# Kernel optimization log

Hardware: AMD Instinct MI355X
Metric: run time of the kernel (lower is better)

## Reference

```python
import jax, jax.numpy as jnp
import numpy as np

N_NODES = 50000
N_EDGES = 800000
F_IN = 64
H = 128
N_CLASSES = 10
NUM_GRAPHS = 512


def setup_inputs() -> dict:
    key = jax.random.key(0)
    ks = jax.random.split(key, 16)
    x = jax.random.normal(ks[0], (N_NODES, F_IN), dtype=jnp.float32)
    edge_index = jax.random.randint(ks[1], (2, N_EDGES), 0, N_NODES, dtype=jnp.int64)
    batch = jnp.sort(jax.random.randint(ks[2], (N_NODES,), 0, NUM_GRAPHS, dtype=jnp.int64))

    def lin(k, fi, fo):
        kw, kb = jax.random.split(k)
        s = 1.0 / np.sqrt(fi)
        return (jax.random.uniform(kw, (fi, fo), jnp.float32, -s, s),
                jax.random.uniform(kb, (fo,), jnp.float32, -s, s))

    W0, b0 = lin(ks[3], F_IN, H)
    W1, b1 = lin(ks[4], H, H)
    W2, b2 = lin(ks[5], H, H)
    mW0, mb0 = lin(ks[6], H, H)
    mW1, mb1 = lin(ks[7], H, H)
    mW2, mb2 = lin(ks[8], H, N_CLASSES)
    return {"x": x, "edge_index": edge_index, "batch": batch,
            "W0": W0, "b0": b0, "W1": W1, "b1": b1, "W2": W2, "b2": b2,
            "mW0": mW0, "mb0": mb0, "mW1": mW1, "mb1": mb1, "mW2": mW2, "mb2": mb2}


def reference(x, edge_index, batch, W0, b0, W1, b1, W2, b2, mW0, mb0, mW1, mb1, mW2, mb2):
    N = x.shape[0]
    loop = jnp.arange(N, dtype=edge_index.dtype)
    src = jnp.concatenate([edge_index[0], loop])  # add self-loops (PyG GCNConv)
    dst = jnp.concatenate([edge_index[1], loop])
    deg = jax.ops.segment_sum(jnp.ones_like(src, jnp.float32), dst, num_segments=N)
    dinv = jnp.where(deg > 0, deg ** -0.5, 0.0)
    norm = dinv[src] * dinv[dst]  # [E+N]

    def gcn(h, W, b):
        h = h @ W                                   # [N, H]
        msg = h[src] * norm[:, None]                # gather [E+N, H]
        return jax.ops.segment_sum(msg, dst, num_segments=N) + b

    h = jax.nn.relu(gcn(x, W0, b0))
    h = jax.nn.relu(gcn(h, W1, b1))
    h = jax.nn.relu(gcn(h, W2, b2))
    g = jax.ops.segment_sum(h, batch, num_segments=NUM_GRAPHS)  # global_add_pool
    g = jax.nn.relu(g @ mW0 + mb0)
    g = jax.nn.relu(g @ mW1 + mb1)
    return g @ mW2 + mb2  # [NUM_GRAPHS, N_CLASSES]
```

## Files before the change

### kernel.cpp

```cpp
#include <hip/hip_runtime.h>
#include <hip/hip_bf16.h>
#include <stdint.h>

#define N_NODES   50000
#define N_EDGES   800000
#define F_IN      64
#define HID       128
#define N_CLASSES 10
#define NUM_GRAPHS 512

#define NBUCK 128
#define BW    391
#define S1B   400
#define CHUNK 2000
#define MCNT  (NBUCK * S1B)
#define PREPB 3125

typedef unsigned int uint32;
typedef __attribute__((ext_vector_type(8))) short bf16x8;
typedef __attribute__((ext_vector_type(4))) float f32x4;

__device__ __forceinline__ float bl(uint32 w) { return __uint_as_float(w << 16); }
__device__ __forceinline__ float bh(uint32 w) { return __uint_as_float(w & 0xffff0000u); }
__device__ __forceinline__ uint32 packbf(float a, float b) {
    uint32 ua = __float_as_uint(a), ub = __float_as_uint(b);
    ua = (ua + 0x7fffu + ((ua >> 16) & 1u)) >> 16;
    ub = (ub + 0x7fffu + ((ub >> 16) & 1u)) >> 16;
    return ua | (ub << 16);
}
__device__ __forceinline__ unsigned short packbf1(float a) {
    uint32 ua = __float_as_uint(a);
    return (unsigned short)((ua + 0x7fffu + ((ua >> 16) & 1u)) >> 16);
}

__global__ __launch_bounds__(256) void prep_hist_kernel(const float4* __restrict__ x, uint2* __restrict__ xb,
                                                        const float* __restrict__ W0, unsigned short* __restrict__ W0t,
                                                        const float* __restrict__ W1, unsigned short* __restrict__ W1t,
                                                        const float* __restrict__ W2, unsigned short* __restrict__ W2t,
                                                        const int* __restrict__ dst, int* __restrict__ bcnt, int E) {
    __shared__ int cnt[NBUCK];
    int blk = blockIdx.x;
    int t = threadIdx.x;
    if (blk < PREPB) {
        int i = blk * 256 + t;
        if (i < N_NODES * F_IN / 4) {
            float4 v = x[i];
            xb[i] = make_uint2(packbf(v.x, v.y), packbf(v.z, v.w));
        }
        if (i < 64 * 128) {
            int k = i >> 7, j = i & 127;
            W0t[j * (64 + 8) + k] = packbf1(W0[i]);
        }
        int i2 = i - 64 * 128;
        if (i2 >= 0 && i2 < 128 * 128) {
            int k = i2 >> 7, j = i2 & 127;
            W1t[j * (128 + 8) + k] = packbf1(W1[i2]);
            W2t[j * (128 + 8) + k] = packbf1(W2[i2]);
        }
    } else {
        int b2 = blk - PREPB;
        if (t < NBUCK) cnt[t] = 0;
        __syncthreads();
        int base = b2 * CHUNK;
        for (int i = t; i < CHUNK; i += 256) {
            int e = base + i;
            if (e < E) atomicAdd(&cnt[(uint32)dst[e] / BW], 1);
        }
        __syncthreads();
        if (t < NBUCK) bcnt[t * S1B + b2] = cnt[t];
    }
}

__global__ __launch_bounds__(256) void scanA_kernel(const int* __restrict__ in,
                                                    int* __restrict__ incl,
                                                    int* __restrict__ bsum, int M) {
    __shared__ int s[256];
    int t = threadIdx.x;
    int i = blockIdx.x * 256 + t;
    int v = (i < M) ? in[i] : 0;
    s[t] = v;
    __syncthreads();
    #pragma unroll
    for (int d = 1; d < 256; d <<= 1) {
        int a = (t >= d) ? s[t - d] : 0;
        __syncthreads();
        s[t] += a;
        __syncthreads();
    }
    if (i < M) incl[i] = s[t];
    if (t == 255) bsum[blockIdx.x] = s[255];
}

__global__ __launch_bounds__(256) void scanB_kernel(int* __restrict__ bsum, int NB) {
    __shared__ int s[256];
    int t = threadIdx.x;
    int v = (t < NB) ? bsum[t] : 0;
    s[t] = v;
    __syncthreads();
    #pragma unroll
    for (int d = 1; d < 256; d <<= 1) {
        int a = (t >= d) ? s[t - d] : 0;
        __syncthreads();
        s[t] += a;
        __syncthreads();
    }
    if (t < NB) bsum[t] = s[t] - v;
}

__global__ __launch_bounds__(256) void bscatter_kernel(const int* __restrict__ src,
                                                       const int* __restrict__ dst,
                                                       const int* __restrict__ incl,
                                                       const int* __restrict__ bsum,
                                                       int2* __restrict__ ebuf, int E) {
    __shared__ int cnt[NBUCK];
    __shared__ int cur[NBUCK];
    int t = threadIdx.x, blk = blockIdx.x;
    if (t < NBUCK) cnt[t] = 0;
    __syncthreads();
    int base = blk * CHUNK;
    for (int i = t; i < CHUNK; i += 256) {
        int e = base + i;
        if (e < E) atomicAdd(&cnt[(uint32)dst[e] / BW], 1);
    }
    __syncthreads();
    if (t < NBUCK) {
        int idx = t * S1B + blk;
        cur[t] = bsum[idx >> 8] + incl[idx] - cnt[t];
    }
    __syncthreads();
    for (int i = t; i < CHUNK; i += 256) {
        int e = base + i;
        if (e < E) {
            int d = dst[e];
            int slot = atomicAdd(&cur[(uint32)d / BW], 1);
            ebuf[slot] = make_int2(src[e], d);
        }
    }
}

__global__ __launch_bounds__(256) void bfinal_kernel(const int2* __restrict__ ebuf,
                                                     const int* __restrict__ bcnt,
                                                     const int* __restrict__ incl,
                                                     const int* __restrict__ bsum,
                                                     int* __restrict__ rowptr,
                                                     float* __restrict__ dinv,
                                                     int2* __restrict__ meta, int E, int N) {
    __shared__ int cnt[392];
    __shared__ int startv[400];
    __shared__ int segt[16];
    int t = threadIdx.x, b = blockIdx.x;

    int bs, be;
    {
        int idx = b * S1B;
        bs = bsum[idx >> 8] + incl[idx] - bcnt[idx];
        if (b + 1 >= NBUCK) be = E;
        else {
            int idx1 = (b + 1) * S1B;
            be = bsum[idx1 >> 8] + incl[idx1] - bcnt[idx1];
        }
    }

    for (int i = t; i < 392; i += 256) cnt[i] = 0;
    __syncthreads();
    for (int i = bs + t; i < be; i += 256) {
        int d = ebuf[i].y;
        atomicAdd(&cnt[d - b * BW], 1);
    }
    __syncthreads();

    if (t < 16) {
        int run = 0;
        #pragma unroll
        for (int k = 0; k < 25; k++) {
            int idx = t * 25 + k;
            int c = (idx < 391) ? cnt[idx] : 0;
            startv[idx] = run;
            run += c;
        }
        segt[t] = run;
    }
    __syncthreads();
    if (t == 0) {
        int run = 0;
        #pragma unroll
        for (int j = 0; j < 16; j++) { int s = segt[j]; segt[j] = run; run += s; }
    }
    __syncthreads();
    for (int l = t; l < 391; l += 256) startv[l] += segt[l / 25] + bs;
    __syncthreads();

    int locN = N - b * BW; if (locN > BW) locN = BW;
    for (int l = t; l < locN; l += 256) {
        int g = b * BW + l;
        rowptr[g + 1] = startv[l] + cnt[l];
        dinv[g] = rsqrtf((float)(cnt[l] + 1));
    }
    if (b == 0 && t == 0) rowptr[0] = 0;
    __syncthreads();

    for (int i = bs + t; i < be; i += 256) {
        int2 sd = ebuf[i];
        int slot = atomicAdd(&startv[sd.y - b * BW], 1);
        meta[slot] = sd;
    }
}

__global__ __launch_bounds__(256) void norm_kernel(int2* __restrict__ meta,
                                                   const float* __restrict__ dinv, int E) {
    int i = blockIdx.x * 256 + threadIdx.x;
    if (i < E) {
        int2 m = meta[i];
        meta[i] = make_int2(m.x, __float_as_int(dinv[m.x] * dinv[m.y]));
    }
}

__global__ __launch_bounds__(256) void spmm128_kernel(const int* __restrict__ rowptr,
                                                      const int2* __restrict__ meta,
                                                      const float* __restrict__ dinv,
                                                      const unsigned short* __restrict__ Hin,
                                                      unsigned short* __restrict__ Hout, int N) {
    int wave = threadIdx.x >> 6;
    int lane = threadIdx.x & 63;
    int node = blockIdx.x * 4 + wave;
    if (node >= N) return;
    int q   = lane >> 4;
    int sub = lane & 15;

    const uint4* Hv = (const uint4*)Hin;
    float di = dinv[node];
    float sn = di * di;

    float acc[8];
    if (q == 0) {
        uint4 s = Hv[(size_t)node * 16 + sub];
        acc[0] = sn * bl(s.x); acc[1] = sn * bh(s.x);
        acc[2] = sn * bl(s.y); acc[3] = sn * bh(s.y);
        acc[4] = sn * bl(s.z); acc[5] = sn * bh(s.z);
        acc[6] = sn * bl(s.w); acc[7] = sn * bh(s.w);
    } else {
        #pragma unroll
        for (int v = 0; v < 8; v++) acc[v] = 0.f;
    }

    int e0 = rowptr[node];
    int e1 = rowptr[node + 1];
    for (int e = e0; e < e1; e += 16) {
        int i0 = e + q;
        int i1 = e + 4 + q;
        int i2 = e + 8 + q;
        int i3 = e + 12 + q;
        int2 m0 = (i0 < e1) ? meta[i0] : make_int2(0, 0);
        int2 m1 = (i1 < e1) ? meta[i1] : make_int2(0, 0);
        int2 m2 = (i2 < e1) ? meta[i2] : make_int2(0, 0);
        int2 m3 = (i3 < e1) ? meta[i3] : make_int2(0, 0);
        float n0 = __int_as_float(m0.y);
        float n1 = __int_as_float(m1.y);
        float n2 = __int_as_float(m2.y);
        float n3 = __int_as_float(m3.y);
        uint4 r0 = Hv[(size_t)m0.x * 16 + sub];
        uint4 r1 = Hv[(size_t)m1.x * 16 + sub];
        uint4 r2 = Hv[(size_t)m2.x * 16 + sub];
        uint4 r3 = Hv[(size_t)m3.x * 16 + sub];
        acc[0] = fmaf(n0, bl(r0.x), acc[0]); acc[1] = fmaf(n0, bh(r0.x), acc[1]);
        acc[2] = fmaf(n0, bl(r0.y), acc[2]); acc[3] = fmaf(n0, bh(r0.y), acc[3]);
        acc[4] = fmaf(n0, bl(r0.z), acc[4]); acc[5] = fmaf(n0, bh(r0.z), acc[5]);
        acc[6] = fmaf(n0, bl(r0.w), acc[6]); acc[7] = fmaf(n0, bh(r0.w), acc[7]);
        acc[0] = fmaf(n1, bl(r1.x), acc[0]); acc[1] = fmaf(n1, bh(r1.x), acc[1]);
        acc[2] = fmaf(n1, bl(r1.y), acc[2]); acc[3] = fmaf(n1, bh(r1.y), acc[3]);
        acc[4] = fmaf(n1, bl(r1.z), acc[4]); acc[5] = fmaf(n1, bh(r1.z), acc[5]);
        acc[6] = fmaf(n1, bl(r1.w), acc[6]); acc[7] = fmaf(n1, bh(r1.w), acc[7]);
        acc[0] = fmaf(n2, bl(r2.x), acc[0]); acc[1] = fmaf(n2, bh(r2.x), acc[1]);
        acc[2] = fmaf(n2, bl(r2.y), acc[2]); acc[3] = fmaf(n2, bh(r2.y), acc[3]);
        acc[4] = fmaf(n2, bl(r2.z), acc[4]); acc[5] = fmaf(n2, bh(r2.z), acc[5]);
        acc[6] = fmaf(n2, bl(r2.w), acc[6]); acc[7] = fmaf(n2, bh(r2.w), acc[7]);
        acc[0] = fmaf(n3, bl(r3.x), acc[0]); acc[1] = fmaf(n3, bh(r3.x), acc[1]);
        acc[2] = fmaf(n3, bl(r3.y), acc[2]); acc[3] = fmaf(n3, bh(r3.y), acc[3]);
        acc[4] = fmaf(n3, bl(r3.z), acc[4]); acc[5] = fmaf(n3, bh(r3.z), acc[5]);
        acc[6] = fmaf(n3, bl(r3.w), acc[6]); acc[7] = fmaf(n3, bh(r3.w), acc[7]);
    }

    #pragma unroll
    for (int v = 0; v < 8; v++) {
        acc[v] += __shfl_xor(acc[v], 16);
        acc[v] += __shfl_xor(acc[v], 32);
    }

    if (q == 0) {
        uint4 o;
        o.x = packbf(acc[0], acc[1]);
        o.y = packbf(acc[2], acc[3]);
        o.z = packbf(acc[4], acc[5]);
        o.w = packbf(acc[6], acc[7]);
        ((uint4*)Hout)[(size_t)node * 16 + sub] = o;
    }
}

__global__ __launch_bounds__(256) void spmm64_kernel(const int* __restrict__ rowptr,
                                                     const int2* __restrict__ meta,
                                                     const float* __restrict__ dinv,
                                                     const unsigned short* __restrict__ Hin,
                                                     unsigned short* __restrict__ Hout, int N) {
    int wave = threadIdx.x >> 6;
    int lane = threadIdx.x & 63;
    int node = blockIdx.x * 4 + wave;
    if (node >= N) return;
    int oct = lane >> 3;
    int sub = lane & 7;

    const uint4* Hv = (const uint4*)Hin;
    float di = dinv[node];
    float sn = di * di;

    float acc[8];
    if (oct == 0) {
        uint4 s = Hv[(size_t)node * 8 + sub];
        acc[0] = sn * bl(s.x); acc[1] = sn * bh(s.x);
        acc[2] = sn * bl(s.y); acc[3] = sn * bh(s.y);
        acc[4] = sn * bl(s.z); acc[5] = sn * bh(s.z);
        acc[6] = sn * bl(s.w); acc[7] = sn * bh(s.w);
    } else {
        #pragma unroll
        for (int v = 0; v < 8; v++) acc[v] = 0.f;
    }

    int e0 = rowptr[node];
    int e1 = rowptr[node + 1];
    for (int e = e0; e < e1; e += 16) {
        int i0 = e + oct;
        int i1 = e + 8 + oct;
        int2 m0 = (i0 < e1) ? meta[i0] : make_int2(0, 0);
        int2 m1 = (i1 < e1) ? meta[i1] : make_int2(0, 0);
        float n0 = __int_as_float(m0.y);
        float n1 = __int_as_float(m1.y);
        uint4 r0 = Hv[(size_t)m0.x * 8 + sub];
        uint4 r1 = Hv[(size_t)m1.x * 8 + sub];
        acc[0] = fmaf(n0, bl(r0.x), acc[0]); acc[1] = fmaf(n0, bh(r0.x), acc[1]);
        acc[2] = fmaf(n0, bl(r0.y), acc[2]); acc[3] = fmaf(n0, bh(r0.y), acc[3]);
        acc[4] = fmaf(n0, bl(r0.z), acc[4]); acc[5] = fmaf(n0, bh(r0.z), acc[5]);
        acc[6] = fmaf(n0, bl(r0.w), acc[6]); acc[7] = fmaf(n0, bh(r0.w), acc[7]);
        acc[0] = fmaf(n1, bl(r1.x), acc[0]); acc[1] = fmaf(n1, bh(r1.x), acc[1]);
        acc[2] = fmaf(n1, bl(r1.y), acc[2]); acc[3] = fmaf(n1, bh(r1.y), acc[3]);
        acc[4] = fmaf(n1, bl(r1.z), acc[4]); acc[5] = fmaf(n1, bh(r1.z), acc[5]);
        acc[6] = fmaf(n1, bl(r1.w), acc[6]); acc[7] = fmaf(n1, bh(r1.w), acc[7]);
    }

    #pragma unroll
    for (int v = 0; v < 8; v++) {
        acc[v] += __shfl_xor(acc[v], 8);
        acc[v] += __shfl_xor(acc[v], 16);
        acc[v] += __shfl_xor(acc[v], 32);
    }

    if (oct == 0) {
        uint4 o;
        o.x = packbf(acc[0], acc[1]);
        o.y = packbf(acc[2], acc[3]);
        o.z = packbf(acc[4], acc[5]);
        o.w = packbf(acc[6], acc[7]);
        ((uint4*)Hout)[(size_t)node * 8 + sub] = o;
    }
}

template <int K>
__global__ __launch_bounds__(256) void gemm_mfma_kernel(const unsigned short* __restrict__ A,
                                                        const unsigned short* __restrict__ Wt,
                                                        const float* __restrict__ bias,
                                                        unsigned short* __restrict__ out,
                                                        int N) {
    constexpr int KP = K + 8;
    __shared__ unsigned short Wl[128 * KP];

    int t = threadIdx.x;
    constexpr int TOT = 128 * KP * 2 / 16;
    #pragma unroll
    for (int i = 0; i < (TOT + 255) / 256; i++) {
        int idx = i * 256 + t;
        if (idx < TOT) ((uint4*)Wl)[idx] = ((const uint4*)Wt)[idx];
    }
    __syncthreads();

    int wave = t >> 6;
    int lane = t & 63;
    int rowBase = blockIdx.x * 128 + wave * 32;
    int r0 = rowBase + (lane & 15);
    int r1 = r0 + 16;
    if (r0 >= N) r0 = N - 1;
    if (r1 >= N) r1 = N - 1;
    int kchunk = lane >> 4;
    int colSub = lane & 15;

    f32x4 acc0[8], acc1[8];
    #pragma unroll
    for (int i = 0; i < 8; i++) { acc0[i] = (f32x4)0.0f; acc1[i] = (f32x4)0.0f; }

    #pragma unroll
    for (int s = 0; s < K / 32; s++) {
        bf16x8 a0 = *(const bf16x8*)(A + (size_t)r0 * K + s * 32 + kchunk * 8);
        bf16x8 a1 = *(const bf16x8*)(A + (size_t)r1 * K + s * 32 + kchunk * 8);
        #pragma unroll
        for (int tl = 0; tl < 8; tl++) {
            bf16x8 b = *(const bf16x8*)(Wl + (tl * 16 + colSub) * KP + s * 32 + kchunk * 8);
            acc0[tl] = __builtin_amdgcn_mfma_f32_16x16x32_bf16(a0, b, acc0[tl], 0, 0, 0);
            acc1[tl] = __builtin_amdgcn_mfma_f32_16x16x32_bf16(a1, b, acc1[tl], 0, 0, 0);
        }
    }

    int rowOff = (lane >> 4) * 4;
    #pragma unroll
    for (int tl = 0; tl < 8; tl++) {
        int col = tl * 16 + colSub;
        float bv = bias[col];
        #pragma unroll
        for (int r = 0; r < 4; r++) {
            int rowA = rowBase + rowOff + r;
            int rowB = rowA + 16;
            if (rowA < N) {
                float v = fmaxf(acc0[tl][r] + bv, 0.f);
                out[(size_t)rowA * 128 + col] = packbf1(v);
            }
            if (rowB < N) {
                float v = fmaxf(acc1[tl][r] + bv, 0.f);
                out[(size_t)rowB * 128 + col] = packbf1(v);
            }
        }
    }
}

__device__ __forceinline__ int lowerb(const int* a, int n, int v) {
    int lo = 0, hi = n;
    while (lo < hi) {
        int m = (lo + hi) >> 1;
        if (a[m] < v) lo = m + 1; else hi = m;
    }
    return lo;
}

__global__ __launch_bounds__(256) void pool_mlp_kernel(const unsigned short* __restrict__ H,
                                                       const int* __restrict__ batch,
                                                       const float* __restrict__ mW0, const float* __restrict__ mb0,
                                                       const float* __restrict__ mW1, const float* __restrict__ mb1,
                                                       const float* __restrict__ mW2, const float* __restrict__ mb2,
                                                       float* __restrict__ out, int N) {
    int b = blockIdx.x;
    int t = threadIdx.x;
    int jw = t & 63;
    int g  = t >> 6;
    int lo = lowerb(batch, N, b);
    int hi = lowerb(batch, N, b + 1);

    const uint32* Hu = (const uint32*)H;
    float f0 = 0.f, f1 = 0.f;
    for (int n = lo + g; n < hi; n += 4) {
        uint32 v = Hu[(size_t)n * 64 + jw];
        f0 += bl(v);
        f1 += bh(v);
    }

    __shared__ float part[4][HID];
    __shared__ float l0[HID];
    __shared__ float l1[HID];
    part[g][jw * 2 + 0] = f0;
    part[g][jw * 2 + 1] = f1;
    __syncthreads();
    if (t < 128) l0[t] = part[0][t] + part[1][t] + part[2][t] + part[3][t];
    __syncthreads();

    if (t < 128) {
        int j = t;
        float a0 = mb0[j], a1 = 0.f, a2 = 0.f, a3 = 0.f;
        #pragma unroll 4
        for (int k = 0; k < HID; k += 4) {
            a0 = fmaf(l0[k + 0], mW0[(k + 0) * HID + j], a0);
            a1 = fmaf(l0[k + 1], mW0[(k + 1) * HID + j], a1);
            a2 = fmaf(l0[k + 2], mW0[(k + 2) * HID + j], a2);
            a3 = fmaf(l0[k + 3], mW0[(k + 3) * HID + j], a3);
        }
        l1[j] = fmaxf((a0 + a1) + (a2 + a3), 0.f);
    }
    __syncthreads();

    float c = 0.f;
    if (t < 128) {
        int j = t;
        float a0 = mb1[j], a1 = 0.f, a2 = 0.f, a3 = 0.f;
        #pragma unroll 4
        for (int k = 0; k < HID; k += 4) {
            a0 = fmaf(l1[k + 0], mW1[(k + 0) * HID + j], a0);
            a1 = fmaf(l1[k + 1], mW1[(k + 1) * HID + j], a1);
            a2 = fmaf(l1[k + 2], mW1[(k + 2) * HID + j], a2);
            a3 = fmaf(l1[k + 3], mW1[(k + 3) * HID + j], a3);
        }
        c = fmaxf((a0 + a1) + (a2 + a3), 0.f);
    }
    __syncthreads();
    if (t < 128) l0[t] = c;
    __syncthreads();

    if (t < N_CLASSES) {
        float a0 = mb2[t], a1 = 0.f, a2 = 0.f, a3 = 0.f;
        #pragma unroll 4
        for (int k = 0; k < HID; k += 4) {
            a0 = fmaf(l0[k + 0], mW2[(k + 0) * N_CLASSES + t], a0);
            a1 = fmaf(l0[k + 1], mW2[(k + 1) * N_CLASSES + t], a1);
            a2 = fmaf(l0[k + 2], mW2[(k + 2) * N_CLASSES + t], a2);
            a3 = fmaf(l0[k + 3], mW2[(k + 3) * N_CLASSES + t], a3);
        }
        out[b * N_CLASSES + t] = (a0 + a1) + (a2 + a3);
    }
}

extern "C" void kernel_launch(void* const* d_in, const int* in_sizes, int n_in,
                              void* d_out, int out_size, void* d_ws, size_t ws_size,
                              hipStream_t stream) {
    const float* x     = (const float*)d_in[0];
    const int*   ei    = (const int*)d_in[1];
    const int*   batch = (const int*)d_in[2];
    const float* W0  = (const float*)d_in[3];
    const float* b0  = (const float*)d_in[4];
    const float* W1  = (const float*)d_in[5];
    const float* b1  = (const float*)d_in[6];
    const float* W2  = (const float*)d_in[7];
    const float* b2  = (const float*)d_in[8];
    const float* mW0 = (const float*)d_in[9];
    const float* mb0 = (const float*)d_in[10];
    const float* mW1 = (const float*)d_in[11];
    const float* mb1 = (const float*)d_in[12];
    const float* mW2 = (const float*)d_in[13];
    const float* mb2 = (const float*)d_in[14];
    float* out = (float*)d_out;

    const int N = N_NODES, E = N_EDGES;
    const int* src = ei;
    const int* dst = ei + E;

    char* w = (char*)d_ws;
    auto alloc = [&](size_t bytes) -> void* {
        void* p = (void*)w;
        w += (bytes + 255) & ~(size_t)255;
        return p;
    };
    int*   rowptr = (int*)alloc((size_t)(N + 1) * 4);
    int2*  ebuf   = (int2*)alloc((size_t)E * 8);
    int2*  meta   = (int2*)alloc((size_t)E * 8);
    int*   bcnt   = (int*)alloc((size_t)MCNT * 4);
    int*   incl   = (int*)alloc((size_t)MCNT * 4);
    int*   bsum   = (int*)alloc(256 * 4);
    float* dinv   = (float*)alloc((size_t)N * 4);
    unsigned short* xb   = (unsigned short*)alloc((size_t)N * F_IN * 2);
    unsigned short* bufA = (unsigned short*)alloc((size_t)N * HID * 2);
    unsigned short* bufB = (unsigned short*)alloc((size_t)N * HID * 2);
    unsigned short* W0t  = (unsigned short*)alloc((size_t)128 * (64 + 8) * 2);
    unsigned short* W1t  = (unsigned short*)alloc((size_t)128 * (128 + 8) * 2);
    unsigned short* W2t  = (unsigned short*)alloc((size_t)128 * (128 + 8) * 2);

    const int EB   = (E + 255) / 256;
    const int SPB  = (N + 3) / 4;
    const int GB   = (N + 127) / 128;
    const int SCB  = (MCNT + 255) / 256;

    prep_hist_kernel<<<PREPB + S1B, 256, 0, stream>>>((const float4*)x, (uint2*)xb,
                                                      W0, W0t, W1, W1t, W2, W2t,
                                                      dst, bcnt, E);
    scanA_kernel<<<SCB, 256, 0, stream>>>(bcnt, incl, bsum, MCNT);
    scanB_kernel<<<1, 256, 0, stream>>>(bsum, SCB);
    bscatter_kernel<<<S1B, 256, 0, stream>>>(src, dst, incl, bsum, ebuf, E);
    bfinal_kernel<<<NBUCK, 256, 0, stream>>>(ebuf, bcnt, incl, bsum, rowptr, dinv, meta, E, N);
    norm_kernel<<<EB, 256, 0, stream>>>(meta, dinv, E);

    spmm64_kernel<<<SPB, 256, 0, stream>>>(rowptr, meta, dinv, xb, bufA, N);
    gemm_mfma_kernel<64><<<GB, 256, 0, stream>>>(bufA, W0t, b0, bufB, N);

    spmm128_kernel<<<SPB, 256, 0, stream>>>(rowptr, meta, dinv, bufB, bufA, N);
    gemm_mfma_kernel<128><<<GB, 256, 0, stream>>>(bufA, W1t, b1, bufB, N);

    spmm128_kernel<<<SPB, 256, 0, stream>>>(rowptr, meta, dinv, bufB, bufA, N);
    gemm_mfma_kernel<128><<<GB, 256, 0, stream>>>(bufA, W2t, b2, bufB, N);

    pool_mlp_kernel<<<NUM_GRAPHS, 256, 0, stream>>>(bufB, batch, mW0, mb0, mW1, mb1, mW2, mb2, out, N);
}
```

Baseline: 217.1 us.

## Pack edge metadata into 32 bits and fold top-level scan into consumers

Edge buffers shrink from int2 to a single uint32, holding a 16-bit source index with either the 16-bit destination or a bf16 normalization weight, which halves edge traffic in the CSR build and in every SpMM pass. The separate single-block scanB launch is removed, and each bscatter/bfinal block now redoes the small top-level scan locally. bfinal stages its bucket's sorted edges in LDS so global writes become contiguous. Packing node ids into 16 bits is only valid for fewer than 65536 nodes, and storing the norm as bf16 loses precision.

After: 201.0 us. -7.4%, faster.

```diff
diff --git a/kernel.cpp b/kernel.cpp
--- a/kernel.cpp
+++ b/kernel.cpp
@@ -14,7 +14,9 @@
 #define S1B   400
 #define CHUNK 2000
 #define MCNT  (NBUCK * S1B)
+#define SCB   (MCNT / 256)
 #define PREPB 3125
+#define MAXB  8192
 
 typedef unsigned int uint32;
 typedef __attribute__((ext_vector_type(8))) short bf16x8;
@@ -73,7 +75,7 @@
 
 __global__ __launch_bounds__(256) void scanA_kernel(const int* __restrict__ in,
                                                     int* __restrict__ incl,
-                                                    int* __restrict__ bsum, int M) {
+                                                    int* __restrict__ bsum_raw, int M) {
     __shared__ int s[256];
     int t = threadIdx.x;
     int i = blockIdx.x * 256 + t;
@@ -88,33 +90,38 @@
         __syncthreads();
     }
     if (i < M) incl[i] = s[t];
-    if (t == 255) bsum[blockIdx.x] = s[255];
-}
-
-__global__ __launch_bounds__(256) void scanB_kernel(int* __restrict__ bsum, int NB) {
-    __shared__ int s[256];
-    int t = threadIdx.x;
-    int v = (t < NB) ? bsum[t] : 0;
-    s[t] = v;
+    if (t == 255) bsum_raw[blockIdx.x] = s[255];
+}
+
+__device__ __forceinline__ void local_top_scan(const int* __restrict__ bsum_raw, int* exs, int t) {
+    int bv = (t < SCB) ? bsum_raw[t] : 0;
+    exs[t] = bv;
     __syncthreads();
     #pragma unroll
     for (int d = 1; d < 256; d <<= 1) {
-        int a = (t >= d) ? s[t - d] : 0;
+        int a = (t >= d) ? exs[t - d] : 0;
         __syncthreads();
-        s[t] += a;
+        exs[t] += a;
         __syncthreads();
     }
-    if (t < NB) bsum[t] = s[t] - v;
+    int iv = exs[t];
+    __syncthreads();
+    exs[t] = iv - bv;
+    __syncthreads();
 }
 
 __global__ __launch_bounds__(256) void bscatter_kernel(const int* __restrict__ src,
                                                        const int* __restrict__ dst,
                                                        const int* __restrict__ incl,
-                                                       const int* __restrict__ bsum,
-                                                       int2* __restrict__ ebuf, int E) {
+                                                       const int* __restrict__ bsum_raw,
+                                                       uint32* __restrict__ ebuf, int E) {
+    __shared__ int exs[256];
     __shared__ int cnt[NBUCK];
     __shared__ int cur[NBUCK];
     int t = threadIdx.x, blk = blockIdx.x;
+
+    local_top_scan(bsum_raw, exs, t);
+
     if (t < NBUCK) cnt[t] = 0;
     __syncthreads();
     int base = blk * CHUNK;
@@ -125,7 +132,7 @@
     __syncthreads();
     if (t < NBUCK) {
         int idx = t * S1B + blk;
-        cur[t] = bsum[idx >> 8] + incl[idx] - cnt[t];
+        cur[t] = exs[idx >> 8] + incl[idx] - cnt[t];
     }
     __syncthreads();
     for (int i = t; i < CHUNK; i += 256) {
@@ -133,38 +140,43 @@
         if (e < E) {
             int d = dst[e];
             int slot = atomicAdd(&cur[(uint32)d / BW], 1);
-            ebuf[slot] = make_int2(src[e], d);
-        }
-    }
-}
-
-__global__ __launch_bounds__(256) void bfinal_kernel(const int2* __restrict__ ebuf,
+            ebuf[slot] = (uint32)src[e] | ((uint32)d << 16);
+        }
+    }
+}
+
+__global__ __launch_bounds__(256) void bfinal_kernel(const uint32* __restrict__ ebuf,
                                                      const int* __restrict__ bcnt,
                                                      const int* __restrict__ incl,
-                                                     const int* __restrict__ bsum,
+                                                     const int* __restrict__ bsum_raw,
                                                      int* __restrict__ rowptr,
                                                      float* __restrict__ dinv,
-                                                     int2* __restrict__ meta, int E, int N) {
+                                                     uint32* __restrict__ meta, int E, int N) {
+    __shared__ int exs[256];
     __shared__ int cnt[392];
     __shared__ int startv[400];
     __shared__ int segt[16];
+    __shared__ uint32 smeta[MAXB];
     int t = threadIdx.x, b = blockIdx.x;
+
+    local_top_scan(bsum_raw, exs, t);
 
     int bs, be;
     {
         int idx = b * S1B;
-        bs = bsum[idx >> 8] + incl[idx] - bcnt[idx];
+        bs = exs[idx >> 8] + incl[idx] - bcnt[idx];
         if (b + 1 >= NBUCK) be = E;
         else {
             int idx1 = (b + 1) * S1B;
-            be = bsum[idx1 >> 8] + incl[idx1] - bcnt[idx1];
-        }
-    }
+            be = exs[idx1 >> 8] + incl[idx1] - bcnt[idx1];
+        }
+    }
+    int sz = be - bs;
 
     for (int i = t; i < 392; i += 256) cnt[i] = 0;
     __syncthreads();
     for (int i = bs + t; i < be; i += 256) {
-        int d = ebuf[i].y;
+        uint32 d = ebuf[i] >> 16;
         atomicAdd(&cnt[d - b * BW], 1);
     }
     __syncthreads();
@@ -187,36 +199,47 @@
         for (int j = 0; j < 16; j++) { int s = segt[j]; segt[j] = run; run += s; }
     }
     __syncthreads();
-    for (int l = t; l < 391; l += 256) startv[l] += segt[l / 25] + bs;
+    for (int l = t; l < 391; l += 256) startv[l] += segt[l / 25];
     __syncthreads();
 
     int locN = N - b * BW; if (locN > BW) locN = BW;
     for (int l = t; l < locN; l += 256) {
         int g = b * BW + l;
-        rowptr[g + 1] = startv[l] + cnt[l];
+        rowptr[g + 1] = bs + startv[l] + cnt[l];
         dinv[g] = rsqrtf((float)(cnt[l] + 1));
     }
     if (b == 0 && t == 0) rowptr[0] = 0;
     __syncthreads();
 
-    for (int i = bs + t; i < be; i += 256) {
-        int2 sd = ebuf[i];
-        int slot = atomicAdd(&startv[sd.y - b * BW], 1);
-        meta[slot] = sd;
-    }
-}
-
-__global__ __launch_bounds__(256) void norm_kernel(int2* __restrict__ meta,
+    if (sz <= MAXB) {
+        for (int i = bs + t; i < be; i += 256) {
+            uint32 v = ebuf[i];
+            int slot = atomicAdd(&startv[(v >> 16) - b * BW], 1);
+            smeta[slot] = v;
+        }
+        __syncthreads();
+        for (int i = t; i < sz; i += 256) meta[bs + i] = smeta[i];
+    } else {
+        for (int i = bs + t; i < be; i += 256) {
+            uint32 v = ebuf[i];
+            int slot = atomicAdd(&startv[(v >> 16) - b * BW], 1);
+            meta[bs + slot] = v;
+        }
+    }
+}
+
+__global__ __launch_bounds__(256) void norm_kernel(uint32* __restrict__ meta,
                                                    const float* __restrict__ dinv, int E) {
     int i = blockIdx.x * 256 + threadIdx.x;
     if (i < E) {
-        int2 m = meta[i];
-        meta[i] = make_int2(m.x, __float_as_int(dinv[m.x] * dinv[m.y]));
+        uint32 m = meta[i];
+        uint32 s = m & 0xffffu, d = m >> 16;
+        meta[i] = s | ((uint32)packbf1(dinv[s] * dinv[d]) << 16);
     }
 }
 
 __global__ __launch_bounds__(256) void spmm128_kernel(const int* __restrict__ rowptr,
-                                                      const int2* __restrict__ meta,
+                                                      const uint32* __restrict__ meta,
                                                       const float* __restrict__ dinv,
                                                       const unsigned short* __restrict__ Hin,
                                                       unsigned short* __restrict__ Hout, int N) {
@@ -250,18 +273,18 @@
         int i1 = e + 4 + q;
         int i2 = e + 8 + q;
         int i3 = e + 12 + q;
-        int2 m0 = (i0 < e1) ? meta[i0] : make_int2(0, 0);
-        int2 m1 = (i1 < e1) ? meta[i1] : make_int2(0, 0);
-        int2 m2 = (i2 < e1) ? meta[i2] : make_int2(0, 0);
-        int2 m3 = (i3 < e1) ? meta[i3] : make_int2(0, 0);
-        float n0 = __int_as_float(m0.y);
-        float n1 = __int_as_float(m1.y);
-        float n2 = __int_as_float(m2.y);
-        float n3 = __int_as_float(m3.y);
-        uint4 r0 = Hv[(size_t)m0.x * 16 + sub];
-        uint4 r1 = Hv[(size_t)m1.x * 16 + sub];
-        uint4 r2 = Hv[(size_t)m2.x * 16 + sub];
-        uint4 r3 = Hv[(size_t)m3.x * 16 + sub];
+        uint32 m0 = (i0 < e1) ? meta[i0] : 0u;
+        uint32 m1 = (i1 < e1) ? meta[i1] : 0u;
+        uint32 m2 = (i2 < e1) ? meta[i2] : 0u;
+        uint32 m3 = (i3 < e1) ? meta[i3] : 0u;
+        float n0 = bh(m0);
+        float n1 = bh(m1);
+        float n2 = bh(m2);
+        float n3 = bh(m3);
+        uint4 r0 = Hv[(size_t)(m0 & 0xffffu) * 16 + sub];
+        uint4 r1 = Hv[(size_t)(m1 & 0xffffu) * 16 + sub];
+        uint4 r2 = Hv[(size_t)(m2 & 0xffffu) * 16 + sub];
+        uint4 r3 = Hv[(size_t)(m3 & 0xffffu) * 16 + sub];
         acc[0] = fmaf(n0, bl(r0.x), acc[0]); acc[1] = fmaf(n0, bh(r0.x), acc[1]);
         acc[2] = fmaf(n0, bl(r0.y), acc[2]); acc[3] = fmaf(n0, bh(r0.y), acc[3]);
         acc[4] = fmaf(n0, bl(r0.z), acc[4]); acc[5] = fmaf(n0, bh(r0.z), acc[5]);
@@ -297,7 +320,7 @@
 }
 
 __global__ __launch_bounds__(256) void spmm64_kernel(const int* __restrict__ rowptr,
-                                                     const int2* __restrict__ meta,
+                                                     const uint32* __restrict__ meta,
                                                      const float* __restrict__ dinv,
                                                      const unsigned short* __restrict__ Hin,
                                                      unsigned short* __restrict__ Hout, int N) {
@@ -329,12 +352,12 @@
     for (int e = e0; e < e1; e += 16) {
         int i0 = e + oct;
         int i1 = e + 8 + oct;
-        int2 m0 = (i0 < e1) ? meta[i0] : make_int2(0, 0);
-        int2 m1 = (i1 < e1) ? meta[i1] : make_int2(0, 0);
-        float n0 = __int_as_float(m0.y);
-        float n1 = __int_as_float(m1.y);
-        uint4 r0 = Hv[(size_t)m0.x * 8 + sub];
-        uint4 r1 = Hv[(size_t)m1.x * 8 + sub];
+        uint32 m0 = (i0 < e1) ? meta[i0] : 0u;
+        uint32 m1 = (i1 < e1) ? meta[i1] : 0u;
+        float n0 = bh(m0);
+        float n1 = bh(m1);
+        uint4 r0 = Hv[(size_t)(m0 & 0xffffu) * 8 + sub];
+        uint4 r1 = Hv[(size_t)(m1 & 0xffffu) * 8 + sub];
         acc[0] = fmaf(n0, bl(r0.x), acc[0]); acc[1] = fmaf(n0, bh(r0.x), acc[1]);
         acc[2] = fmaf(n0, bl(r0.y), acc[2]); acc[3] = fmaf(n0, bh(r0.y), acc[3]);
         acc[4] = fmaf(n0, bl(r0.z), acc[4]); acc[5] = fmaf(n0, bh(r0.z), acc[5]);
@@ -540,13 +563,13 @@
         w += (bytes + 255) & ~(size_t)255;
         return p;
     };
-    int*   rowptr = (int*)alloc((size_t)(N + 1) * 4);
-    int2*  ebuf   = (int2*)alloc((size_t)E * 8);
-    int2*  meta   = (int2*)alloc((size_t)E * 8);
-    int*   bcnt   = (int*)alloc((size_t)MCNT * 4);
-    int*   incl   = (int*)alloc((size_t)MCNT * 4);
-    int*   bsum   = (int*)alloc(256 * 4);
-    float* dinv   = (float*)alloc((size_t)N * 4);
+    int*    rowptr   = (int*)alloc((size_t)(N + 1) * 4);
+    uint32* ebuf     = (uint32*)alloc((size_t)E * 4);
+    uint32* meta     = (uint32*)alloc((size_t)E * 4);
+    int*    bcnt     = (int*)alloc((size_t)MCNT * 4);
+    int*    incl     = (int*)alloc((size_t)MCNT * 4);
+    int*    bsum_raw = (int*)alloc(256 * 4);
+    float*  dinv     = (float*)alloc((size_t)N * 4);
     unsigned short* xb   = (unsigned short*)alloc((size_t)N * F_IN * 2);
     unsigned short* bufA = (unsigned short*)alloc((size_t)N * HID * 2);
     unsigned short* bufB = (unsigned short*)alloc((size_t)N * HID * 2);
@@ -557,15 +580,13 @@
     const int EB   = (E + 255) / 256;
     const int SPB  = (N + 3) / 4;
     const int GB   = (N + 127) / 128;
-    const int SCB  = (MCNT + 255) / 256;
 
     prep_hist_kernel<<<PREPB + S1B, 256, 0, stream>>>((const float4*)x, (uint2*)xb,
                                                       W0, W0t, W1, W1t, W2, W2t,
                                                       dst, bcnt, E);
-    scanA_kernel<<<SCB, 256, 0, stream>>>(bcnt, incl, bsum, MCNT);
-    scanB_kernel<<<1, 256, 0, stream>>>(bsum, SCB);
-    bscatter_kernel<<<S1B, 256, 0, stream>>>(src, dst, incl, bsum, ebuf, E);
-    bfinal_kernel<<<NBUCK, 256, 0, stream>>>(ebuf, bcnt, incl, bsum, rowptr, dinv, meta, E, N);
+    scanA_kernel<<<SCB, 256, 0, stream>>>(bcnt, incl, bsum_raw, MCNT);
+    bscatter_kernel<<<S1B, 256, 0, stream>>>(src, dst, incl, bsum_raw, ebuf, E);
+    bfinal_kernel<<<NBUCK, 256, 0, stream>>>(ebuf, bcnt, incl, bsum_raw, rowptr, dinv, meta, E, N);
     norm_kernel<<<EB, 256, 0, stream>>>(meta, dinv, E);
 
     spmm64_kernel<<<SPB, 256, 0, stream>>>(rowptr, meta, dinv, xb, bufA, N);
```
